# Kernel optimization log

Hardware: AMD Instinct MI355X
Metric: run time of the kernel (lower is better)

The kernel has to match this reference:

```python
import jax, jax.numpy as jnp
import numpy as np

N_NODES = 50000
N_EDGES = 1600000
C = 128
N_LAYERS = 8


def setup_inputs() -> dict:
    key = jax.random.key(0)
    ks = jax.random.split(key, 10)
    s = lambda fan_in: 1.0 / np.sqrt(fan_in)
    return {
        "x": jax.random.normal(ks[0], (N_NODES, C), dtype=jnp.float32),
        "edge_index": jax.random.randint(ks[1], (2, N_EDGES), 0, N_NODES, dtype=jnp.int32),
        "convs_W": jax.random.normal(ks[2], (N_LAYERS, C, C), dtype=jnp.float32) * s(C),
        "convs_b": jax.random.normal(ks[3], (N_LAYERS, C), dtype=jnp.float32) * s(C),
        "fc0_W": jax.random.normal(ks[4], (2 * C, C), dtype=jnp.float32) * s(2 * C),
        "fc0_b": jax.random.normal(ks[5], (C,), dtype=jnp.float32) * s(2 * C),
        "fc1_W": jax.random.normal(ks[6], (C, C), dtype=jnp.float32) * s(C),
        "fc1_b": jax.random.normal(ks[7], (C,), dtype=jnp.float32) * s(C),
        "fc2_W": jax.random.normal(ks[8], (C, 1), dtype=jnp.float32) * s(C),
        "fc2_b": jax.random.normal(ks[9], (1,), dtype=jnp.float32) * s(C),
    }


def reference(x, edge_index, convs_W, convs_b, fc0_W, fc0_b, fc1_W, fc1_b, fc2_W, fc2_b):
    N = x.shape[0]
    row, col = edge_index[0], edge_index[1]

    # GCNConv default: add self-loops, symmetric D^{-1/2}(A+I)D^{-1/2} normalization
    loops = jnp.arange(N, dtype=row.dtype)
    row_sl = jnp.concatenate([row, loops])  # source of message
    col_sl = jnp.concatenate([col, loops])  # target of aggregation
    deg = jax.ops.segment_sum(jnp.ones(row_sl.shape[0], x.dtype), col_sl, num_segments=N)
    dis = jnp.where(deg > 0, jax.lax.rsqrt(deg), 0.0)
    norm = dis[row_sl] * dis[col_sl]  # [E + N]

    def gcn_conv(h, W, b):
        h = h @ W                                  # [N, C]
        msg = h[row_sl] * norm[:, None]            # [E+N, C] gather + scale
        agg = jax.ops.segment_sum(msg, col_sl, num_segments=N)
        return agg + b

    h = jax.nn.relu(gcn_conv(x, convs_W[0], convs_b[0]))
    for i in range(1, convs_W.shape[0]):
        h = jax.nn.relu(gcn_conv(h, convs_W[i], convs_b[i]) + h)

    # edge MLP classifier on cat([h[src], h[dst]])
    e = jnp.concatenate([h[row], h[col]], axis=1)  # [E, 2C]
    e = jax.nn.relu(e @ fc0_W + fc0_b)
    e = jax.nn.relu(e @ fc1_W + fc1_b)
    return e @ fc2_W + fc2_b                       # [E, 1]
```

## Files before the change

### kernel.cpp

```cpp
#include <hip/hip_runtime.h>

#define C 128

typedef __attribute__((ext_vector_type(4))) float float4v;
typedef _Float16 half8v __attribute__((ext_vector_type(8)));
typedef _Float16 half4v __attribute__((ext_vector_type(4)));
typedef _Float16 half2v __attribute__((ext_vector_type(2)));

__device__ __forceinline__ _Float16* swzh(_Float16* base, int row, int chunk) {
  return base + row * 128 + ((chunk ^ (row & 15)) << 3);
}

__global__ void k_degree(const int* __restrict__ col, int* __restrict__ cnt, int E) {
  int e = blockIdx.x * blockDim.x + threadIdx.x;
  if (e < E) atomicAdd(&cnt[col[e]], 1);
}

__global__ void k_scan(const int* __restrict__ cnt, float* __restrict__ dis,
                       int* __restrict__ indptr, int* __restrict__ cursor, int N) {
  __shared__ int sb[1024];
  int t = threadIdx.x;
  int chunk = (N + 1023) >> 10;
  int lo = t * chunk, hi = min(lo + chunk, N);
  int sum = 0;
  for (int i = lo; i < hi; ++i) sum += cnt[i];
  sb[t] = sum;
  __syncthreads();
  for (int off = 1; off < 1024; off <<= 1) {
    int v = (t >= off) ? sb[t - off] : 0;
    __syncthreads();
    sb[t] += v;
    __syncthreads();
  }
  int run = sb[t] - sum;
  for (int i = lo; i < hi; ++i) {
    indptr[i] = run; cursor[i] = run;
    dis[i] = rsqrtf((float)(cnt[i] + 1));
    run += cnt[i];
  }
  if (lo < N && hi == N) indptr[N] = run;
}

__global__ void k_csrfill(const int* __restrict__ row, const int* __restrict__ col,
                          const float* __restrict__ dis, int* __restrict__ cursor,
                          int2* __restrict__ emeta, int2* __restrict__ epair,
                          int* __restrict__ inv, int E) {
  int e = blockIdx.x * blockDim.x + threadIdx.x;
  if (e >= E) return;
  int r = row[e], c = col[e];
  int pos = atomicAdd(&cursor[c], 1);
  float nrm = dis[r] * dis[c];
  emeta[pos] = make_int2(r, __float_as_int(nrm));
  epair[pos] = make_int2(r, c);
  inv[e] = pos;
}

__global__ void k_cvt(const float* __restrict__ x, _Float16* __restrict__ xh, int n4) {
  int i = blockIdx.x * 256 + threadIdx.x;
  if (i >= n4) return;
  float4 v = ((const float4*)x)[i];
  half4v o = {(_Float16)v.x, (_Float16)v.y, (_Float16)v.z, (_Float16)v.w};
  *(half4v*)(xh + i * 4) = o;
}

__global__ void k_prepwf(const float* __restrict__ W1, _Float16* __restrict__ Wf) {
  int idx = blockIdx.x * 256 + threadIdx.x;
  int e = idx & 7, lane = (idx >> 3) & 63, j = (idx >> 9) & 7, kk = idx >> 12;
  int n = j * 16 + (lane & 15);
  int k = (kk * 4 + (lane >> 4)) * 8 + e;
  Wf[idx] = (_Float16)W1[k * C + n];
}

__global__ void k_prepw2(const float* __restrict__ convs_W,
                         const float* __restrict__ fc0_W,
                         _Float16* __restrict__ Wfh, _Float16* __restrict__ Wfl) {
  int g = blockIdx.x * 256 + threadIdx.x;
  int mat = g >> 14, idx = g & 16383;
  int e = idx & 7, lane = (idx >> 3) & 63, j = (idx >> 9) & 7, kk = idx >> 12;
  int n = j * 16 + (lane & 15);
  int k = (kk * 4 + (lane >> 4)) * 8 + e;
  const float* src = (mat < 8) ? convs_W + ((size_t)mat << 14)
                               : fc0_W + ((size_t)(mat - 8) << 14);
  float v = src[k * C + n];
  _Float16 h = (_Float16)v;
  Wfh[g] = h;
  Wfl[g] = (_Float16)((v - (float)h) * 4096.f);
}

__global__ __launch_bounds__(256)
void k_agg(const _Float16* __restrict__ h, const int* __restrict__ indptr,
           const int2* __restrict__ emeta, const float* __restrict__ dis,
           _Float16* __restrict__ agg, int N) {
  int w = (blockIdx.x * 256 + threadIdx.x) >> 6;
  int lane = threadIdx.x & 63;
  if (w >= N) return;
  int g16 = lane >> 4, c8 = lane & 15;
  int s = indptr[w], e = indptr[w + 1];
  float acc[8];
#pragma unroll
  for (int j = 0; j < 8; ++j) acc[j] = 0.f;

  int i = s;
  for (; i + 16 <= e; i += 16) {
    int2 m[4];
#pragma unroll
    for (int u = 0; u < 4; ++u) m[u] = emeta[i + u * 4 + g16];
    half8v hv[4];
#pragma unroll
    for (int u = 0; u < 4; ++u)
      hv[u] = *(const half8v*)(h + (size_t)m[u].x * C + c8 * 8);
#pragma unroll
    for (int u = 0; u < 4; ++u) {
      float nn = __int_as_float(m[u].y);
#pragma unroll
      for (int j = 0; j < 8; ++j) acc[j] += nn * (float)hv[u][j];
    }
  }
  for (; i + 4 <= e; i += 4) {
    int2 m = emeta[i + g16];
    half8v hv = *(const half8v*)(h + (size_t)m.x * C + c8 * 8);
    float nn = __int_as_float(m.y);
#pragma unroll
    for (int j = 0; j < 8; ++j) acc[j] += nn * (float)hv[j];
  }
  if (i < e) {
    int idx = i + g16;
    int2 m = make_int2(w, 0);
    if (idx < e) m = emeta[idx];
    half8v hv = *(const half8v*)(h + (size_t)m.x * C + c8 * 8);
    float nn = __int_as_float(m.y);
#pragma unroll
    for (int j = 0; j < 8; ++j) acc[j] += nn * (float)hv[j];
  }
#pragma unroll
  for (int j = 0; j < 8; ++j) {
    acc[j] += __shfl_xor(acc[j], 16, 64);
    acc[j] += __shfl_xor(acc[j], 32, 64);
  }
  if (lane < 16) {
    float dv = dis[w];
    float dv2 = dv * dv;
    half8v hs = *(const half8v*)(h + (size_t)w * C + lane * 8);
    half8v o;
#pragma unroll
    for (int j = 0; j < 8; ++j) o[j] = (_Float16)(acc[j] + dv2 * (float)hs[j]);
    *(half8v*)(agg + (size_t)w * C + lane * 8) = o;
  }
}

__global__ __launch_bounds__(256, 4)
void k_gemm_f16(const _Float16* __restrict__ A,
                const _Float16* __restrict__ Wfh, const _Float16* __restrict__ Wfl,
                const float* __restrict__ bias, const _Float16* __restrict__ skip,
                _Float16* __restrict__ out, int M, int relu) {
  int t = threadIdx.x;
  int r0 = blockIdx.x * 64;
  int w = t >> 6, lane = t & 63;
  int m0 = w * 16, lm = lane & 15, lq = lane >> 4;
  int row = r0 + m0 + lm;
  if (row >= M) row = M - 1;
  const _Float16* Ar = A + (size_t)row * C;

  float4v acch[8], accl[8];
#pragma unroll
  for (int j = 0; j < 8; ++j) {
    acch[j] = (float4v){0.f, 0.f, 0.f, 0.f};
    accl[j] = (float4v){0.f, 0.f, 0.f, 0.f};
  }
#pragma unroll
  for (int kk = 0; kk < 4; ++kk) {
    half8v a = *(const half8v*)(Ar + kk * 32 + lq * 8);
#pragma unroll
    for (int j = 0; j < 8; ++j) {
      int fi = ((kk * 8 + j) * 64 + lane) << 3;
      half8v bh = *(const half8v*)(Wfh + fi);
      half8v bl = *(const half8v*)(Wfl + fi);
      acch[j] = __builtin_amdgcn_mfma_f32_16x16x32_f16(a, bh, acch[j], 0, 0, 0);
      accl[j] = __builtin_amdgcn_mfma_f32_16x16x32_f16(a, bl, accl[j], 0, 0, 0);
    }
  }
#pragma unroll
  for (int j = 0; j < 8; ++j) {
    int n = j * 16 + lm;
    float bv = bias ? bias[n] : 0.f;
#pragma unroll
    for (int r = 0; r < 4; ++r) {
      int m = r0 + m0 + lq * 4 + r;
      if (m >= M) continue;
      float v = acch[j][r] + accl[j][r] * (1.f / 4096.f) + bv;
      if (skip) v += (float)skip[(size_t)m * C + n];
      if (relu) v = fmaxf(v, 0.f);
      out[(size_t)m * C + n] = (_Float16)v;
    }
  }
}

__global__ __launch_bounds__(256, 6)
void k_edge(const _Float16* __restrict__ P, const _Float16* __restrict__ Q,
            const int2* __restrict__ epair, const _Float16* __restrict__ Wf,
            const float* __restrict__ b1, const float* __restrict__ w2,
            const float* __restrict__ b2, float* __restrict__ tmpout, int E) {
  __shared__ __align__(16) _Float16 Et[64 * 128];
  int t = threadIdx.x;
  int p0 = blockIdx.x * 64;
  {
    int el = t >> 2, p4 = t & 3;
    int p = p0 + el;
    if (p >= E) p = E - 1;
    int2 rc = epair[p];
    const _Float16* Pp = P + (size_t)rc.x * C + p4 * 32;
    const _Float16* Qp = Q + (size_t)rc.y * C + p4 * 32;
#pragma unroll
    for (int i = 0; i < 4; ++i) {
      half8v a = *(const half8v*)(Pp + 8 * i);
      half8v b = *(const half8v*)(Qp + 8 * i);
      half8v sum = a + b;
      half8v o;
#pragma unroll
      for (int j = 0; j < 8; ++j) {
        _Float16 v = sum[j];
        o[j] = (v > (_Float16)0.f) ? v : (_Float16)0.f;
      }
      *(half8v*)swzh(Et, el, p4 * 4 + i) = o;
    }
  }
  __syncthreads();

  int w = t >> 6, lane = t & 63;
  int m0 = w * 16;
  int lm = lane & 15, lq = lane >> 4;
  float4v acc[8];
#pragma unroll
  for (int j = 0; j < 8; ++j) acc[j] = (float4v){0.f, 0.f, 0.f, 0.f};

#pragma unroll
  for (int kk = 0; kk < 4; ++kk) {
    int ch = kk * 4 + lq;
    half8v ah = *(const half8v*)swzh(Et, m0 + lm, ch);
#pragma unroll
    for (int j = 0; j < 8; ++j) {
      half8v b = *(const half8v*)(Wf + (((kk * 8 + j) * 64 + lane) << 3));
      acc[j] = __builtin_amdgcn_mfma_f32_16x16x32_f16(ah, b, acc[j], 0, 0, 0);
    }
  }

  float partv[4] = {0.f, 0.f, 0.f, 0.f};
#pragma unroll
  for (int j = 0; j < 8; ++j) {
    int n = j * 16 + lm;
    float b1v = b1[n], w2v = w2[n];
#pragma unroll
    for (int r = 0; r < 4; ++r) {
      float e2 = fmaxf(acc[j][r] + b1v, 0.f);
      partv[r] = fmaf(e2, w2v, partv[r]);
    }
  }
#pragma unroll
  for (int off = 1; off < 16; off <<= 1) {
#pragma unroll
    for (int r = 0; r < 4; ++r) partv[r] += __shfl_xor(partv[r], off, 64);
  }
  if (lm == 0) {
    float bb = b2[0];
#pragma unroll
    for (int r = 0; r < 4; ++r) {
      int p = p0 + m0 + lq * 4 + r;
      if (p < E) tmpout[p] = partv[r] + bb;
    }
  }
}

__global__ void k_perm(const float* __restrict__ tmp, const int* __restrict__ inv,
                       float* __restrict__ out, int E) {
  int e = blockIdx.x * 256 + threadIdx.x;
  if (e < E) out[e] = tmp[inv[e]];
}

extern "C" void kernel_launch(void* const* d_in, const int* in_sizes, int n_in,
                              void* d_out, int out_size, void* d_ws, size_t ws_size,
                              hipStream_t stream) {
  const float* x       = (const float*)d_in[0];
  const int*   ei      = (const int*)d_in[1];
  const float* convs_W = (const float*)d_in[2];
  const float* convs_b = (const float*)d_in[3];
  const float* fc0_W   = (const float*)d_in[4];
  const float* fc0_b   = (const float*)d_in[5];
  const float* fc1_W   = (const float*)d_in[6];
  const float* fc1_b   = (const float*)d_in[7];
  const float* fc2_W   = (const float*)d_in[8];
  const float* fc2_b   = (const float*)d_in[9];
  float* out = (float*)d_out;

  const int N = in_sizes[0] / C;
  const int E = in_sizes[1] / 2;
  const int L = in_sizes[2] / (C * C);
  const int* row = ei;
  const int* col = ei + E;

  char* wp = (char*)d_ws;
  auto carve = [&](size_t bytes) {
    char* p = wp; wp += (bytes + 255) & ~(size_t)255; return p;
  };
  int*      cnt    = (int*)carve((size_t)N * 4);
  int*      indptr = (int*)carve((size_t)(N + 1) * 4);
  int*      cursor = (int*)carve((size_t)N * 4);
  float*    dis    = (float*)carve((size_t)N * 4);
  int2*     emeta  = (int2*)carve((size_t)E * 8);
  int2*     epair  = (int2*)carve((size_t)E * 8);
  int*      inv    = (int*)carve((size_t)E * 4);
  float*    tmpout = (float*)carve((size_t)E * 4);
  _Float16* Wf     = (_Float16*)carve((size_t)C * C * 2);
  _Float16* Wfh    = (_Float16*)carve((size_t)10 * C * C * 2);
  _Float16* Wfl    = (_Float16*)carve((size_t)10 * C * C * 2);
  _Float16* xh     = (_Float16*)carve((size_t)N * C * 2);
  _Float16* h0     = (_Float16*)carve((size_t)N * C * 2);
  _Float16* h1     = (_Float16*)carve((size_t)N * C * 2);
  _Float16* aggb   = (_Float16*)carve((size_t)N * C * 2);
  _Float16* Pm     = (_Float16*)carve((size_t)N * C * 2);
  _Float16* Qm     = (_Float16*)carve((size_t)N * C * 2);

  hipMemsetAsync(cnt, 0, (size_t)N * 4, stream);
  k_degree<<<(E + 255) / 256, 256, 0, stream>>>(col, cnt, E);
  k_scan<<<1, 1024, 0, stream>>>(cnt, dis, indptr, cursor, N);
  k_csrfill<<<(E + 255) / 256, 256, 0, stream>>>(row, col, dis, cursor,
                                                 emeta, epair, inv, E);
  k_prepwf<<<C * C / 256, 256, 0, stream>>>(fc1_W, Wf);
  k_prepw2<<<10 * C * C / 256, 256, 0, stream>>>(convs_W, fc0_W, Wfh, Wfl);
  k_cvt<<<(N * C / 4 + 255) / 256, 256, 0, stream>>>(x, xh, N * C / 4);

  int aggBlocks  = (N * 64 + 255) / 256;
  int gemmBlocks = (N + 63) / 64;
  const int MSZ = C * C;

  k_agg<<<aggBlocks, 256, 0, stream>>>(xh, indptr, emeta, dis, aggb, N);
  k_gemm_f16<<<gemmBlocks, 256, 0, stream>>>(aggb, Wfh, Wfl, convs_b,
                                             nullptr, h0, N, 1);
  _Float16* hcur = h0; _Float16* hoth = h1;
  for (int l = 1; l < L; ++l) {
    k_agg<<<aggBlocks, 256, 0, stream>>>(hcur, indptr, emeta, dis, aggb, N);
    k_gemm_f16<<<gemmBlocks, 256, 0, stream>>>(aggb, Wfh + (size_t)l * MSZ,
                                               Wfl + (size_t)l * MSZ,
                                               convs_b + (size_t)l * C, hcur,
                                               hoth, N, 1);
    _Float16* tmp = hcur; hcur = hoth; hoth = tmp;
  }
  k_gemm_f16<<<gemmBlocks, 256, 0, stream>>>(hcur, Wfh + (size_t)8 * MSZ,
                                             Wfl + (size_t)8 * MSZ, nullptr,
                                             nullptr, Pm, N, 0);
  k_gemm_f16<<<gemmBlocks, 256, 0, stream>>>(hcur, Wfh + (size_t)9 * MSZ,
                                             Wfl + (size_t)9 * MSZ, fc0_b,
                                             nullptr, Qm, N, 0);
  k_edge<<<(E + 63) / 64, 256, 0, stream>>>(Pm, Qm, epair, Wf, fc1_b,
                                            fc2_W, fc2_b, tmpout, E);
  k_perm<<<(E + 255) / 256, 256, 0, stream>>>(tmpout, inv, out, E);
}
```

Before: 1.231 ms.

## Partition aggregation into source-node chunks for L2 locality of gathered features

Result: slower. 2.000 ms (+62.4%).

```diff
diff --git a/kernel.cpp b/kernel.cpp
--- a/kernel.cpp
+++ b/kernel.cpp
@@ -1,27 +1,39 @@
 #include <hip/hip_runtime.h>
 
 #define C 128
+#define NCH 4
 
 typedef __attribute__((ext_vector_type(4))) float float4v;
 typedef _Float16 half8v __attribute__((ext_vector_type(8)));
 typedef _Float16 half4v __attribute__((ext_vector_type(4)));
-typedef _Float16 half2v __attribute__((ext_vector_type(2)));
 
 __device__ __forceinline__ _Float16* swzh(_Float16* base, int row, int chunk) {
   return base + row * 128 + ((chunk ^ (row & 15)) << 3);
 }
 
-__global__ void k_degree(const int* __restrict__ col, int* __restrict__ cnt, int E) {
+__global__ void k_degree(const int* __restrict__ row, const int* __restrict__ col,
+                         int* __restrict__ cntc, int E, int N, int CH) {
   int e = blockIdx.x * blockDim.x + threadIdx.x;
-  if (e < E) atomicAdd(&cnt[col[e]], 1);
-}
-
-__global__ void k_scan(const int* __restrict__ cnt, float* __restrict__ dis,
-                       int* __restrict__ indptr, int* __restrict__ cursor, int N) {
+  if (e >= E) return;
+  int c = row[e] / CH;
+  atomicAdd(&cntc[c * N + col[e]], 1);
+}
+
+__global__ void k_dis(const int* __restrict__ cntc, float* __restrict__ dis, int N) {
+  int i = blockIdx.x * 256 + threadIdx.x;
+  if (i >= N) return;
+  int d = 0;
+#pragma unroll
+  for (int c = 0; c < NCH; ++c) d += cntc[c * N + i];
+  dis[i] = rsqrtf((float)(d + 1));
+}
+
+__global__ void k_scan(const int* __restrict__ cnt, int* __restrict__ indptr,
+                       int* __restrict__ cursor, int M) {
   __shared__ int sb[1024];
   int t = threadIdx.x;
-  int chunk = (N + 1023) >> 10;
-  int lo = t * chunk, hi = min(lo + chunk, N);
+  int chunk = (M + 1023) >> 10;
+  int lo = t * chunk, hi = min(lo + chunk, M);
   int sum = 0;
   for (int i = lo; i < hi; ++i) sum += cnt[i];
   sb[t] = sum;
@@ -35,20 +47,20 @@
   int run = sb[t] - sum;
   for (int i = lo; i < hi; ++i) {
     indptr[i] = run; cursor[i] = run;
-    dis[i] = rsqrtf((float)(cnt[i] + 1));
     run += cnt[i];
   }
-  if (lo < N && hi == N) indptr[N] = run;
+  if (lo < M && hi == M) indptr[M] = run;
 }
 
 __global__ void k_csrfill(const int* __restrict__ row, const int* __restrict__ col,
                           const float* __restrict__ dis, int* __restrict__ cursor,
                           int2* __restrict__ emeta, int2* __restrict__ epair,
-                          int* __restrict__ inv, int E) {
+                          int* __restrict__ inv, int E, int N, int CH) {
   int e = blockIdx.x * blockDim.x + threadIdx.x;
   if (e >= E) return;
   int r = row[e], c = col[e];
-  int pos = atomicAdd(&cursor[c], 1);
+  int ch = r / CH;
+  int pos = atomicAdd(&cursor[ch * N + c], 1);
   float nrm = dis[r] * dis[c];
   emeta[pos] = make_int2(r, __float_as_int(nrm));
   epair[pos] = make_int2(r, c);
@@ -88,14 +100,16 @@
 }
 
 __global__ __launch_bounds__(256)
-void k_agg(const _Float16* __restrict__ h, const int* __restrict__ indptr,
-           const int2* __restrict__ emeta, const float* __restrict__ dis,
-           _Float16* __restrict__ agg, int N) {
+void k_aggc(const _Float16* __restrict__ h, const int* __restrict__ indptr,
+            const int2* __restrict__ emeta, const float* __restrict__ dis,
+            float* __restrict__ aggf, _Float16* __restrict__ aggh,
+            int N, int chunk, int first, int last) {
   int w = (blockIdx.x * 256 + threadIdx.x) >> 6;
   int lane = threadIdx.x & 63;
   if (w >= N) return;
   int g16 = lane >> 4, c8 = lane & 15;
-  int s = indptr[w], e = indptr[w + 1];
+  int base = chunk * N + w;
+  int s = indptr[base], e = indptr[base + 1];
   float acc[8];
 #pragma unroll
   for (int j = 0; j < 8; ++j) acc[j] = 0.f;
@@ -138,13 +152,33 @@
     acc[j] += __shfl_xor(acc[j], 32, 64);
   }
   if (lane < 16) {
-    float dv = dis[w];
-    float dv2 = dv * dv;
-    half8v hs = *(const half8v*)(h + (size_t)w * C + lane * 8);
-    half8v o;
-#pragma unroll
-    for (int j = 0; j < 8; ++j) o[j] = (_Float16)(acc[j] + dv2 * (float)hs[j]);
-    *(half8v*)(agg + (size_t)w * C + lane * 8) = o;
+    float* af = aggf + (size_t)w * C + lane * 8;
+    float vals[8];
+    if (first) {
+      float dv = dis[w];
+      float dv2 = dv * dv;
+      half8v hs = *(const half8v*)(h + (size_t)w * C + lane * 8);
+#pragma unroll
+      for (int j = 0; j < 8; ++j) vals[j] = dv2 * (float)hs[j];
+    } else {
+      float4v v0 = __builtin_nontemporal_load((const float4v*)af);
+      float4v v1 = __builtin_nontemporal_load((const float4v*)(af + 4));
+      vals[0] = v0[0]; vals[1] = v0[1]; vals[2] = v0[2]; vals[3] = v0[3];
+      vals[4] = v1[0]; vals[5] = v1[1]; vals[6] = v1[2]; vals[7] = v1[3];
+    }
+#pragma unroll
+    for (int j = 0; j < 8; ++j) vals[j] += acc[j];
+    if (last) {
+      half8v o;
+#pragma unroll
+      for (int j = 0; j < 8; ++j) o[j] = (_Float16)vals[j];
+      *(half8v*)(aggh + (size_t)w * C + lane * 8) = o;
+    } else {
+      float4v v0 = {vals[0], vals[1], vals[2], vals[3]};
+      float4v v1 = {vals[4], vals[5], vals[6], vals[7]};
+      __builtin_nontemporal_store(v0, (float4v*)af);
+      __builtin_nontemporal_store(v1, (float4v*)(af + 4));
+    }
   }
 }
 
@@ -296,34 +330,37 @@
   const int L = in_sizes[2] / (C * C);
   const int* row = ei;
   const int* col = ei + E;
+  const int CH = (N + NCH - 1) / NCH;
 
   char* wp = (char*)d_ws;
   auto carve = [&](size_t bytes) {
     char* p = wp; wp += (bytes + 255) & ~(size_t)255; return p;
   };
-  int*      cnt    = (int*)carve((size_t)N * 4);
-  int*      indptr = (int*)carve((size_t)(N + 1) * 4);
-  int*      cursor = (int*)carve((size_t)N * 4);
-  float*    dis    = (float*)carve((size_t)N * 4);
-  int2*     emeta  = (int2*)carve((size_t)E * 8);
-  int2*     epair  = (int2*)carve((size_t)E * 8);
-  int*      inv    = (int*)carve((size_t)E * 4);
-  float*    tmpout = (float*)carve((size_t)E * 4);
-  _Float16* Wf     = (_Float16*)carve((size_t)C * C * 2);
-  _Float16* Wfh    = (_Float16*)carve((size_t)10 * C * C * 2);
-  _Float16* Wfl    = (_Float16*)carve((size_t)10 * C * C * 2);
-  _Float16* xh     = (_Float16*)carve((size_t)N * C * 2);
-  _Float16* h0     = (_Float16*)carve((size_t)N * C * 2);
-  _Float16* h1     = (_Float16*)carve((size_t)N * C * 2);
-  _Float16* aggb   = (_Float16*)carve((size_t)N * C * 2);
-  _Float16* Pm     = (_Float16*)carve((size_t)N * C * 2);
-  _Float16* Qm     = (_Float16*)carve((size_t)N * C * 2);
-
-  hipMemsetAsync(cnt, 0, (size_t)N * 4, stream);
-  k_degree<<<(E + 255) / 256, 256, 0, stream>>>(col, cnt, E);
-  k_scan<<<1, 1024, 0, stream>>>(cnt, dis, indptr, cursor, N);
-  k_csrfill<<<(E + 255) / 256, 256, 0, stream>>>(row, col, dis, cursor,
-                                                 emeta, epair, inv, E);
+  int*      cntc    = (int*)carve((size_t)NCH * N * 4);
+  int*      indptrc = (int*)carve(((size_t)NCH * N + 1) * 4);
+  int*      cursorc = (int*)carve((size_t)NCH * N * 4);
+  float*    dis     = (float*)carve((size_t)N * 4);
+  int2*     emeta   = (int2*)carve((size_t)E * 8);
+  int2*     epair   = (int2*)carve((size_t)E * 8);
+  int*      inv     = (int*)carve((size_t)E * 4);
+  float*    tmpout  = (float*)carve((size_t)E * 4);
+  _Float16* Wf      = (_Float16*)carve((size_t)C * C * 2);
+  _Float16* Wfh     = (_Float16*)carve((size_t)10 * C * C * 2);
+  _Float16* Wfl     = (_Float16*)carve((size_t)10 * C * C * 2);
+  _Float16* xh      = (_Float16*)carve((size_t)N * C * 2);
+  _Float16* h0      = (_Float16*)carve((size_t)N * C * 2);
+  _Float16* h1      = (_Float16*)carve((size_t)N * C * 2);
+  float*    aggf    = (float*)carve((size_t)N * C * 4);
+  _Float16* aggh    = (_Float16*)carve((size_t)N * C * 2);
+  _Float16* Pm      = (_Float16*)carve((size_t)N * C * 2);
+  _Float16* Qm      = (_Float16*)carve((size_t)N * C * 2);
+
+  hipMemsetAsync(cntc, 0, (size_t)NCH * N * 4, stream);
+  k_degree<<<(E + 255) / 256, 256, 0, stream>>>(row, col, cntc, E, N, CH);
+  k_dis<<<(N + 255) / 256, 256, 0, stream>>>(cntc, dis, N);
+  k_scan<<<1, 1024, 0, stream>>>(cntc, indptrc, cursorc, NCH * N);
+  k_csrfill<<<(E + 255) / 256, 256, 0, stream>>>(row, col, dis, cursorc,
+                                                 emeta, epair, inv, E, N, CH);
   k_prepwf<<<C * C / 256, 256, 0, stream>>>(fc1_W, Wf);
   k_prepw2<<<10 * C * C / 256, 256, 0, stream>>>(convs_W, fc0_W, Wfh, Wfl);
   k_cvt<<<(N * C / 4 + 255) / 256, 256, 0, stream>>>(x, xh, N * C / 4);
@@ -332,17 +369,20 @@
   int gemmBlocks = (N + 63) / 64;
   const int MSZ = C * C;
 
-  k_agg<<<aggBlocks, 256, 0, stream>>>(xh, indptr, emeta, dis, aggb, N);
-  k_gemm_f16<<<gemmBlocks, 256, 0, stream>>>(aggb, Wfh, Wfl, convs_b,
-                                             nullptr, h0, N, 1);
-  _Float16* hcur = h0; _Float16* hoth = h1;
-  for (int l = 1; l < L; ++l) {
-    k_agg<<<aggBlocks, 256, 0, stream>>>(hcur, indptr, emeta, dis, aggb, N);
-    k_gemm_f16<<<gemmBlocks, 256, 0, stream>>>(aggb, Wfh + (size_t)l * MSZ,
+  _Float16* hcur = xh;
+  _Float16* bufA = h0;
+  _Float16* bufB = h1;
+  for (int l = 0; l < L; ++l) {
+    for (int c = 0; c < NCH; ++c)
+      k_aggc<<<aggBlocks, 256, 0, stream>>>(hcur, indptrc, emeta, dis, aggf,
+                                            aggh, N, c, c == 0, c == NCH - 1);
+    _Float16* hout = (l == 0) ? bufA : ((hcur == bufA) ? bufB : bufA);
+    k_gemm_f16<<<gemmBlocks, 256, 0, stream>>>(aggh, Wfh + (size_t)l * MSZ,
                                                Wfl + (size_t)l * MSZ,
-                                               convs_b + (size_t)l * C, hcur,
-                                               hoth, N, 1);
-    _Float16* tmp = hcur; hcur = hoth; hoth = tmp;
+                                               convs_b + (size_t)l * C,
+                                               (l == 0) ? nullptr : hcur,
+                                               hout, N, 1);
+    hcur = hout;
   }
   k_gemm_f16<<<gemmBlocks, 256, 0, stream>>>(hcur, Wfh + (size_t)8 * MSZ,
                                              Wfl + (size_t)8 * MSZ, nullptr,
```
